# Kernel tuning notes

Hardware: AMD Instinct MI355X
Metric: run time of the kernel (lower is better)

The kernel has to match this reference:

```python
import jax, jax.numpy as jnp
import numpy as np

DEPTH, HEADS, DIM_HEAD, DIM, MLP, PATCH_DIM, NP_, NC = 8, 8, 64, 512, 2048, 512, 1024, 2
INNER = HEADS * DIM_HEAD
SCALE = DIM_HEAD ** -0.5
EPS = 1e-5

def layernorm(x, s, b):
    m = x.mean(-1, keepdims=True)
    v = ((x - m) ** 2).mean(-1, keepdims=True)
    return (x - m) * jax.lax.rsqrt(v + EPS) * s + b

def setup_inputs() -> dict:
    key = jax.random.key(0)
    ks = jax.random.split(key, 24)
    g = lambda k, sh, sc=0.02: jax.random.normal(k, sh, dtype=jnp.float32) * sc
    return {
        "img": jax.random.normal(ks[0], (4, NP_, PATCH_DIM), dtype=jnp.float32),
        "embed_w": g(ks[1], (PATCH_DIM, DIM)), "embed_b": jnp.zeros((DIM,), jnp.float32),
        "pos_emb": g(ks[2], (1, NP_ + 1, DIM), 1.0), "cls_token": g(ks[3], (1, 1, DIM), 1.0),
        "ln1_s": jnp.ones((DEPTH, DIM), jnp.float32), "ln1_b": jnp.zeros((DEPTH, DIM), jnp.float32),
        "qkv_w": g(ks[4], (DEPTH, DIM, 3 * INNER)),
        "out_w": g(ks[5], (DEPTH, INNER, DIM)), "out_b": jnp.zeros((DEPTH, DIM), jnp.float32),
        "ln2_s": jnp.ones((DEPTH, DIM), jnp.float32), "ln2_b": jnp.zeros((DEPTH, DIM), jnp.float32),
        "ff_w1": g(ks[6], (DEPTH, DIM, MLP)), "ff_b1": jnp.zeros((DEPTH, MLP), jnp.float32),
        "ff_w2": g(ks[7], (DEPTH, MLP, DIM)), "ff_b2": jnp.zeros((DEPTH, DIM), jnp.float32),
        "head_ln_s": jnp.ones((DIM,), jnp.float32), "head_ln_b": jnp.zeros((DIM,), jnp.float32),
        "head_w": g(ks[8], (DIM, NC)), "head_b": jnp.zeros((NC,), jnp.float32),
    }

def reference(img, embed_w, embed_b, pos_emb, cls_token, ln1_s, ln1_b, qkv_w, out_w, out_b,
              ln2_s, ln2_b, ff_w1, ff_b1, ff_w2, ff_b2, head_ln_s, head_ln_b, head_w, head_b):
    B, N, _ = img.shape
    x = img @ embed_w + embed_b                       # [B, N, DIM]
    cls = jnp.broadcast_to(cls_token, (B, 1, DIM))
    x = jnp.concatenate([cls, x], axis=1) + pos_emb[:, :N + 1]
    for l in range(DEPTH):
        h = layernorm(x, ln1_s[l], ln1_b[l])
        qkv = h @ qkv_w[l]                            # [B, N+1, 3*INNER]
        q, k, v = jnp.split(qkv, 3, axis=-1)
        rh = lambda t: t.reshape(B, N + 1, HEADS, DIM_HEAD).transpose(0, 2, 1, 3)
        q, k, v = rh(q), rh(k), rh(v)                 # [B, H, N+1, Dh]
        dots = jnp.einsum('bhnd,bhmd->bhnm', q, k) * SCALE
        attn = jax.nn.softmax(dots, axis=-1)
        o = jnp.einsum('bhnm,bhmd->bhnd', attn, v)
        o = o.transpose(0, 2, 1, 3).reshape(B, N + 1, INNER)
        x = o @ out_w[l] + out_b[l] + x
        h = layernorm(x, ln2_s[l], ln2_b[l])
        h = jax.nn.gelu(h @ ff_w1[l] + ff_b1[l], approximate=False)
        x = h @ ff_w2[l] + ff_b2[l] + x
    x = x[:, 0]                                       # cls pooling
    x = layernorm(x, head_ln_s, head_ln_b)
    return (jax.nn.sigmoid(x @ head_w + head_b),)
```

## Files before the change

kernel.cpp:

```cpp
#include <hip/hip_runtime.h>
#include <math.h>
#include <stdint.h>

#define NHEADS   8
#define DHEAD    64
#define DIMM     512
#define MLPD     2048
#define NPATCH   1024
#define NTOK     1025
#define BATCH    4
#define ROWS     (BATCH*NTOK)
#define TOKPAD   1088
#define ATT_SCALE 0.125f
#define LN_EPS   1e-5f

typedef __attribute__((ext_vector_type(8))) short short8;
typedef __attribute__((ext_vector_type(4))) float f32x4;

__device__ __forceinline__ unsigned short f2bf(float f) {
  union { float f; unsigned u; } c; c.f = f;
  unsigned u = c.u;
  return (unsigned short)((u + 0x7fffu + ((u >> 16) & 1u)) >> 16);
}

__device__ __forceinline__ float wsum(float v) {
#pragma unroll
  for (int o = 32; o > 0; o >>= 1) v += __shfl_xor(v, o, 64);
  return v;
}

__device__ __forceinline__ void gl_lds16(const void* g, const void* l) {
  __builtin_amdgcn_global_load_lds(
      (const __attribute__((address_space(1))) unsigned int*)(uintptr_t)g,
      (__attribute__((address_space(3))) unsigned int*)(unsigned int)(uintptr_t)l,
      16, 0, 0);
}

template <int TM, int TN, int WR, int WC>
__global__ __launch_bounds__(256) void mgemm_k(
    const unsigned short* __restrict__ A, const unsigned short* __restrict__ Bt,
    const float* __restrict__ bias, const float* __restrict__ res,
    void* __restrict__ Cout, int M, int N, int K, int flags)
{
  constexpr int AF = TM / WR / 16;
  constexpr int BF = TN / WC / 16;
  constexpr int AG = TM / 32;
  constexpr int BG = TN / 32;
  __shared__ unsigned short sA[2][TM * 64];
  __shared__ unsigned short sB[2][TN * 64];
  const int tid = threadIdx.x;
  const int w = tid >> 6, lane = tid & 63;
  const int quad = lane >> 4, l15 = lane & 15;
  const int m0 = blockIdx.y * TM, n0 = blockIdx.x * TN;
  const int wrow = (w / WC) * (TM / WR);
  const int wcol = (w % WC) * (TN / WC);
  const int lrow = lane >> 3;
  const int lkg = (lane & 7) ^ lrow;

  size_t abase[AG], bbase[BG];
#pragma unroll
  for (int g = 0; g < AG; g++) {
    int grp = w * AG + g;
    int ar = m0 + grp * 8 + lrow; ar = ar < M ? ar : M - 1;
    abase[g] = (size_t)ar * K + lkg * 8;
  }
#pragma unroll
  for (int g = 0; g < BG; g++) {
    int grp = w * BG + g;
    int br = n0 + grp * 8 + lrow;
    bbase[g] = (size_t)br * K + lkg * 8;
  }

  auto stage = [&](int k0, int buf) {
#pragma unroll
    for (int g = 0; g < AG; g++)
      gl_lds16(A + abase[g] + k0, &sA[buf][(w * AG + g) * 512]);
#pragma unroll
    for (int g = 0; g < BG; g++)
      gl_lds16(Bt + bbase[g] + k0, &sB[buf][(w * BG + g) * 512]);
  };

  f32x4 acc[AF][BF];
#pragma unroll
  for (int i = 0; i < AF; i++)
#pragma unroll
    for (int j = 0; j < BF; j++) { f32x4 z = {0.f, 0.f, 0.f, 0.f}; acc[i][j] = z; }

  stage(0, 0);
  const int nsteps = K >> 6;
  for (int step = 0; step < nsteps; step++) {
    const int buf = step & 1;
    __syncthreads();
    if (step + 1 < nsteps) stage((step + 1) << 6, buf ^ 1);
#pragma unroll
    for (int kk = 0; kk < 2; kk++) {
      short8 af[AF], bfr[BF];
#pragma unroll
      for (int i = 0; i < AF; i++) {
        int r = wrow + i * 16 + l15;
        af[i] = *(const short8*)&sA[buf][r * 64 + (((kk * 4 + quad) ^ (lane & 7)) << 3)];
      }
#pragma unroll
      for (int j = 0; j < BF; j++) {
        int r = wcol + j * 16 + l15;
        bfr[j] = *(const short8*)&sB[buf][r * 64 + (((kk * 4 + quad) ^ (lane & 7)) << 3)];
      }
#pragma unroll
      for (int i = 0; i < AF; i++)
#pragma unroll
        for (int j = 0; j < BF; j++)
          acc[i][j] = __builtin_amdgcn_mfma_f32_16x16x32_bf16(af[i], bfr[j], acc[i][j], 0, 0, 0);
    }
  }

  const bool do_gelu = flags & 1;
  const bool out_bf  = flags & 2;
#pragma unroll
  for (int i = 0; i < AF; i++) {
#pragma unroll
    for (int rg = 0; rg < 4; rg++) {
      int row = m0 + wrow + i * 16 + quad * 4 + rg;
      if (row >= M) continue;
#pragma unroll
      for (int j = 0; j < BF; j++) {
        int col = n0 + wcol + j * 16 + l15;
        float v = acc[i][j][rg];
        if (bias) v += bias[col];
        if (do_gelu) v = 0.5f * v * (1.0f + erff(v * 0.70710678118654752f));
        if (res) v += res[(size_t)row * N + col];
        if (out_bf) ((unsigned short*)Cout)[(size_t)row * N + col] = f2bf(v);
        else        ((float*)Cout)[(size_t)row * N + col] = v;
      }
    }
  }
}

__global__ __launch_bounds__(256) void vtrans_k(
    const unsigned short* __restrict__ qkv, unsigned short* __restrict__ vT)
{
  __shared__ unsigned short tile[64 * 64];
  const int bh = blockIdx.y, b = bh >> 3, h = bh & 7;
  const int t0 = blockIdx.x * 64;
  const int tid = threadIdx.x;
#pragma unroll
  for (int it = 0; it < 2; ++it) {
    int lin = it * 256 + tid;
    int tok = lin >> 3, dg = lin & 7;
    int gt = t0 + tok; gt = gt < NTOK ? gt : NTOK - 1;
    uint4 v = *(const uint4*)(qkv + (size_t)(b * NTOK + gt) * 1536 + 1024 + h * 64 + dg * 8);
    *(uint4*)&tile[tok * 64 + ((dg ^ (tok & 7)) << 3)] = v;
  }
  __syncthreads();
  unsigned short* outp = vT + ((size_t)bh * 64) * TOKPAD + t0;
#pragma unroll
  for (int it = 0; it < 2; ++it) {
    int lin = it * 256 + tid;
    int d = lin >> 3, tg = lin & 7;
    alignas(16) unsigned short o[8];
#pragma unroll
    for (int j = 0; j < 8; j++) {
      int tok = tg * 8 + j;
      o[j] = tile[tok * 64 + ((((d >> 3) ^ (tok & 7)) & 7) << 3) + (d & 7)];
    }
    *(uint4*)(outp + (size_t)d * TOKPAD + tg * 8) = *(const uint4*)o;
  }
}

__global__ __launch_bounds__(256) void attn_k(
    const unsigned short* __restrict__ qkv, const unsigned short* __restrict__ vT,
    unsigned short* __restrict__ out)
{
  __shared__ unsigned short qs[64 * 64];
  __shared__ unsigned short ps[64 * 64];
  __shared__ unsigned short ks[2][64 * 64];
  __shared__ unsigned short vs[2][64 * 64];
  const int bh = blockIdx.y, b = bh >> 3, h = bh & 7;
  const int q0 = blockIdx.x * 64;
  const int tid = threadIdx.x, w = tid >> 6, lane = tid & 63;
  const int quad = lane >> 4, l15 = lane & 15;
  const int lrow = lane >> 3, lkg = (lane & 7) ^ lrow;
  const unsigned short* qbase = qkv + (size_t)(b * NTOK) * 1536 + h * 64;
  const unsigned short* kbase = qbase + 512;
  const unsigned short* vtb   = vT + (size_t)bh * 64 * TOKPAD;

  auto stage_kv = [&](int c0, int buf) {
#pragma unroll
    for (int g = 0; g < 2; g++) {
      int grp = w * 2 + g;
      int tok = c0 + grp * 8 + lrow; tok = tok < NTOK ? tok : NTOK - 1;
      gl_lds16(kbase + (size_t)tok * 1536 + lkg * 8, &ks[buf][grp * 512]);
      int d = grp * 8 + lrow;
      gl_lds16(vtb + (size_t)d * TOKPAD + c0 + lkg * 8, &vs[buf][grp * 512]);
    }
  };

#pragma unroll
  for (int g = 0; g < 2; g++) {
    int grp = w * 2 + g;
    int tok = q0 + grp * 8 + lrow; tok = tok < NTOK ? tok : NTOK - 1;
    gl_lds16(qbase + (size_t)tok * 1536 + lkg * 8, &qs[grp * 512]);
  }
  stage_kv(0, 0);

  short8 ones;
#pragma unroll
  for (int i = 0; i < 8; i++) ones[i] = (short)0x3F80;

  f32x4 Oa[4];
#pragma unroll
  for (int n = 0; n < 4; n++) { f32x4 z = {0.f, 0.f, 0.f, 0.f}; Oa[n] = z; }
  float mst[4], lst[4];
#pragma unroll
  for (int r = 0; r < 4; r++) { mst[r] = -1e30f; lst[r] = 0.f; }

  const int nchunks = (NTOK + 63) / 64;
  for (int c = 0; c < nchunks; c++) {
    const int c0 = c * 64;
    const int buf = c & 1;
    __syncthreads();
    if (c + 1 < nchunks) stage_kv(c0 + 64, buf ^ 1);

    short8 aq[2];
#pragma unroll
    for (int kk = 0; kk < 2; kk++)
      aq[kk] = *(const short8*)&qs[(w * 16 + l15) * 64 + (((kk * 4 + quad) ^ (lane & 7)) << 3)];
    f32x4 sa[4];
#pragma unroll
    for (int n = 0; n < 4; n++) {
      f32x4 s = {0.f, 0.f, 0.f, 0.f};
#pragma unroll
      for (int kk = 0; kk < 2; kk++) {
        short8 bk = *(const short8*)&ks[buf][(n * 16 + l15) * 64 + (((kk * 4 + quad) ^ (lane & 7)) << 3)];
        s = __builtin_amdgcn_mfma_f32_16x16x32_bf16(aq[kk], bk, s, 0, 0, 0);
      }
      sa[n] = s;
    }

#pragma unroll
    for (int n = 0; n < 4; n++) {
      bool oob = (c0 + n * 16 + l15) >= NTOK;
#pragma unroll
      for (int rg = 0; rg < 4; rg++) {
        float sc = sa[n][rg] * ATT_SCALE;
        sa[n][rg] = oob ? -1e30f : sc;
      }
    }
    float alpha[4];
#pragma unroll
    for (int rg = 0; rg < 4; rg++) {
      float mx = fmaxf(fmaxf(sa[0][rg], sa[1][rg]), fmaxf(sa[2][rg], sa[3][rg]));
#pragma unroll
      for (int o = 1; o < 16; o <<= 1) mx = fmaxf(mx, __shfl_xor(mx, o, 64));
      float nm = fmaxf(mst[rg], mx);
      alpha[rg] = __expf(mst[rg] - nm);
      mst[rg] = nm;
#pragma unroll
      for (int n = 0; n < 4; n++) sa[n][rg] = __expf(sa[n][rg] - nm);
    }

#pragma unroll
    for (int n = 0; n < 4; n++)
#pragma unroll
      for (int rg = 0; rg < 4; rg++) {
        int row = w * 16 + quad * 4 + rg;
        int key = n * 16 + l15;
        ps[row * 64 + ((((key >> 3) ^ (row & 7)) & 7) << 3) + (key & 7)] = f2bf(sa[n][rg]);
      }

    short8 ap[2];
#pragma unroll
    for (int kk = 0; kk < 2; kk++)
      ap[kk] = *(const short8*)&ps[(w * 16 + l15) * 64 + (((kk * 4 + quad) ^ (lane & 7)) << 3)];

    f32x4 lsum = {0.f, 0.f, 0.f, 0.f};
#pragma unroll
    for (int kk = 0; kk < 2; kk++)
      lsum = __builtin_amdgcn_mfma_f32_16x16x32_bf16(ap[kk], ones, lsum, 0, 0, 0);

#pragma unroll
    for (int n = 0; n < 4; n++) {
      f32x4 o = Oa[n];
#pragma unroll
      for (int rg = 0; rg < 4; rg++) o[rg] *= alpha[rg];
#pragma unroll
      for (int kk = 0; kk < 2; kk++) {
        short8 bv = *(const short8*)&vs[buf][(n * 16 + l15) * 64 + (((kk * 4 + quad) ^ (lane & 7)) << 3)];
        o = __builtin_amdgcn_mfma_f32_16x16x32_bf16(ap[kk], bv, o, 0, 0, 0);
      }
      Oa[n] = o;
    }
#pragma unroll
    for (int rg = 0; rg < 4; rg++) lst[rg] = lst[rg] * alpha[rg] + lsum[rg];
  }

#pragma unroll
  for (int n = 0; n < 4; n++)
#pragma unroll
    for (int rg = 0; rg < 4; rg++) {
      int tok = q0 + w * 16 + quad * 4 + rg;
      if (tok < NTOK)
        out[(size_t)(b * NTOK + tok) * DIMM + h * 64 + n * 16 + l15] =
            f2bf(Oa[n][rg] / lst[rg]);
    }
}

__global__ __launch_bounds__(256) void ln_k(
    const float* __restrict__ X, const float* __restrict__ s,
    const float* __restrict__ b, unsigned short* __restrict__ Y, int nrows)
{
  const int w = threadIdx.x >> 6, lane = threadIdx.x & 63;
  const int row = blockIdx.x * 4 + w;
  if (row >= nrows) return;
  const float* x = X + (size_t)row * DIMM;
  float4 v0 = *(const float4*)(x + lane * 8);
  float4 v1 = *(const float4*)(x + lane * 8 + 4);
  float xv[8] = {v0.x, v0.y, v0.z, v0.w, v1.x, v1.y, v1.z, v1.w};
  float sum = 0.f, sq = 0.f;
#pragma unroll
  for (int i = 0; i < 8; i++) { sum += xv[i]; sq += xv[i] * xv[i]; }
  sum = wsum(sum); sq = wsum(sq);
  const float mean = sum * (1.0f / DIMM);
  const float var  = sq * (1.0f / DIMM) - mean * mean;
  const float r    = rsqrtf(var + LN_EPS);
  alignas(16) unsigned short tmp[8];
#pragma unroll
  for (int i = 0; i < 8; i++) {
    int d = lane * 8 + i;
    tmp[i] = f2bf((xv[i] - mean) * r * s[d] + b[d]);
  }
  *(uint4*)&Y[(size_t)row * DIMM + lane * 8] = *(const uint4*)tmp;
}

__global__ __launch_bounds__(256) void assemble_k(
    const float* __restrict__ emb, const float* __restrict__ cls,
    const float* __restrict__ pos, float* __restrict__ X)
{
  int idx = blockIdx.x * 256 + threadIdx.x;
  if (idx >= BATCH * NTOK * DIMM) return;
  int d = idx & (DIMM - 1);
  int t = (idx >> 9) % NTOK;
  int b = idx / (NTOK * DIMM);
  float v = (t == 0) ? cls[d] : emb[((size_t)b * NPATCH + (t - 1)) * DIMM + d];
  X[idx] = v + pos[(size_t)t * DIMM + d];
}

__global__ __launch_bounds__(256) void cast_k(
    const float* __restrict__ X, unsigned short* __restrict__ Y, int n4)
{
  int i = blockIdx.x * 256 + threadIdx.x;
  if (i >= n4) return;
  float4 v = ((const float4*)X)[i];
  alignas(8) unsigned short o[4] = {f2bf(v.x), f2bf(v.y), f2bf(v.z), f2bf(v.w)};
  ((uint2*)Y)[i] = *(const uint2*)o;
}

__global__ __launch_bounds__(256) void tcast_k(
    const float* __restrict__ W, unsigned short* __restrict__ Wt, int K, int N)
{
  __shared__ float t[32][33];
  const size_t off = (size_t)blockIdx.z * K * N;
  W += off; Wt += off;
  int n0 = blockIdx.x * 32, k0 = blockIdx.y * 32;
  int tx = threadIdx.x & 31, ty = threadIdx.x >> 5;
#pragma unroll
  for (int i = 0; i < 4; i++)
    t[ty + 8 * i][tx] = W[(size_t)(k0 + ty + 8 * i) * N + n0 + tx];
  __syncthreads();
#pragma unroll
  for (int i = 0; i < 4; i++) {
    int n = ty + 8 * i;
    Wt[(size_t)(n0 + n) * K + k0 + tx] = f2bf(t[tx][n]);
  }
}

__global__ __launch_bounds__(256) void head_k(
    const float* __restrict__ X, const float* __restrict__ s,
    const float* __restrict__ bln, const float* __restrict__ W,
    const float* __restrict__ bh, float* __restrict__ out)
{
  const int w = threadIdx.x >> 6, lane = threadIdx.x & 63;
  if (w >= BATCH) return;
  const float* x = X + (size_t)w * NTOK * DIMM;
  float4 v0 = *(const float4*)(x + lane * 8);
  float4 v1 = *(const float4*)(x + lane * 8 + 4);
  float xv[8] = {v0.x, v0.y, v0.z, v0.w, v1.x, v1.y, v1.z, v1.w};
  float sum = 0.f, sq = 0.f;
#pragma unroll
  for (int i = 0; i < 8; i++) { sum += xv[i]; sq += xv[i] * xv[i]; }
  sum = wsum(sum); sq = wsum(sq);
  const float mean = sum * (1.0f / DIMM);
  const float var  = sq * (1.0f / DIMM) - mean * mean;
  const float r    = rsqrtf(var + LN_EPS);
  float l0 = 0.f, l1 = 0.f;
#pragma unroll
  for (int i = 0; i < 8; i++) {
    int d = lane * 8 + i;
    float xn = (xv[i] - mean) * r * s[d] + bln[d];
    l0 = fmaf(xn, W[d * 2 + 0], l0);
    l1 = fmaf(xn, W[d * 2 + 1], l1);
  }
  l0 = wsum(l0); l1 = wsum(l1);
  if (lane == 0) {
    out[w * 2 + 0] = 1.0f / (1.0f + expf(-(l0 + bh[0])));
    out[w * 2 + 1] = 1.0f / (1.0f + expf(-(l1 + bh[1])));
  }
}

extern "C" void kernel_launch(void* const* d_in, const int* in_sizes, int n_in,
                              void* d_out, int out_size, void* d_ws, size_t ws_size,
                              hipStream_t stream)
{
  const float* img       = (const float*)d_in[0];
  const float* embed_w   = (const float*)d_in[1];
  const float* embed_b   = (const float*)d_in[2];
  const float* pos_emb   = (const float*)d_in[3];
  const float* cls_token = (const float*)d_in[4];
  const float* ln1_s     = (const float*)d_in[5];
  const float* ln1_b     = (const float*)d_in[6];
  const float* qkv_w     = (const float*)d_in[7];
  const float* out_w     = (const float*)d_in[8];
  const float* out_b     = (const float*)d_in[9];
  const float* ln2_s     = (const float*)d_in[10];
  const float* ln2_b     = (const float*)d_in[11];
  const float* ff_w1     = (const float*)d_in[12];
  const float* ff_b1     = (const float*)d_in[13];
  const float* ff_w2     = (const float*)d_in[14];
  const float* ff_b2     = (const float*)d_in[15];
  const float* head_ln_s = (const float*)d_in[16];
  const float* head_ln_b = (const float*)d_in[17];
  const float* head_w    = (const float*)d_in[18];
  const float* head_b    = (const float*)d_in[19];
  float* out = (float*)d_out;

  char* p = (char*)d_ws;
  auto alloc = [&](size_t bytes) { char* r = p; p += (bytes + 255) & ~(size_t)255; return r; };

  unsigned short* wt_embed = (unsigned short*)alloc((size_t)512 * 512 * 2);
  unsigned short* wt_qkv   = (unsigned short*)alloc((size_t)8 * 1536 * 512 * 2);
  unsigned short* wt_out   = (unsigned short*)alloc((size_t)8 * 512 * 512 * 2);
  unsigned short* wt_ff1   = (unsigned short*)alloc((size_t)8 * 2048 * 512 * 2);
  unsigned short* wt_ff2   = (unsigned short*)alloc((size_t)8 * 512 * 2048 * 2);
  unsigned short* img_bf   = (unsigned short*)alloc((size_t)4096 * 512 * 2);
  float*          x        = (float*)alloc((size_t)ROWS * DIMM * 4);
  unsigned short* h        = (unsigned short*)alloc((size_t)ROWS * DIMM * 2);
  unsigned short* vTb      = (unsigned short*)alloc((size_t)32 * 64 * TOKPAD * 2);
  char*           big      = alloc((size_t)ROWS * MLPD * 2);
  unsigned short* qkvb     = (unsigned short*)big;
  unsigned short* attn_out = (unsigned short*)(big + (size_t)ROWS * 1536 * 2);
  unsigned short* ffh      = (unsigned short*)big;
  float*          embuf    = (float*)big;

  dim3 blk(256);

  cast_k<<<(4096 * 512 / 4 + 255) / 256, blk, 0, stream>>>(img, img_bf, 4096 * 512 / 4);
  tcast_k<<<dim3(16, 16, 1), blk, 0, stream>>>(embed_w, wt_embed, 512, 512);
  tcast_k<<<dim3(48, 16, 8), blk, 0, stream>>>(qkv_w, wt_qkv, 512, 1536);
  tcast_k<<<dim3(16, 16, 8), blk, 0, stream>>>(out_w, wt_out, 512, 512);
  tcast_k<<<dim3(64, 16, 8), blk, 0, stream>>>(ff_w1, wt_ff1, 512, 2048);
  tcast_k<<<dim3(16, 64, 8), blk, 0, stream>>>(ff_w2, wt_ff2, 2048, 512);

  mgemm_k<64, 64, 2, 2><<<dim3(8, 64), blk, 0, stream>>>(
      img_bf, wt_embed, embed_b, nullptr, embuf, 4096, 512, 512, 0);
  assemble_k<<<(BATCH * NTOK * DIMM + 255) / 256, blk, 0, stream>>>(
      embuf, cls_token, pos_emb, x);

  const int mt64 = (ROWS + 63) / 64;
  for (int l = 0; l < 8; l++) {
    ln_k<<<(ROWS + 3) / 4, blk, 0, stream>>>(
        x, ln1_s + l * DIMM, ln1_b + l * DIMM, h, ROWS);
    mgemm_k<64, 128, 1, 4><<<dim3(12, mt64), blk, 0, stream>>>(
        h, wt_qkv + (size_t)l * 1536 * 512, nullptr, nullptr,
        qkvb, ROWS, 1536, 512, 2);
    vtrans_k<<<dim3(17, 32), blk, 0, stream>>>(qkvb, vTb);
    attn_k<<<dim3(17, 32), blk, 0, stream>>>(qkvb, vTb, attn_out);
    mgemm_k<64, 64, 2, 2><<<dim3(8, mt64), blk, 0, stream>>>(
        attn_out, wt_out + (size_t)l * 512 * 512, out_b + l * DIMM, x,
        x, ROWS, 512, 512, 0);
    ln_k<<<(ROWS + 3) / 4, blk, 0, stream>>>(
        x, ln2_s + l * DIMM, ln2_b + l * DIMM, h, ROWS);
    mgemm_k<64, 128, 1, 4><<<dim3(16, mt64), blk, 0, stream>>>(
        h, wt_ff1 + (size_t)l * 2048 * 512, ff_b1 + l * MLPD, nullptr,
        ffh, ROWS, 2048, 512, 1 | 2);
    mgemm_k<64, 64, 2, 2><<<dim3(8, mt64), blk, 0, stream>>>(
        ffh, wt_ff2 + (size_t)l * 512 * 2048, ff_b2 + l * DIMM, x,
        x, ROWS, 512, 2048, 0);
  }

  head_k<<<1, blk, 0, stream>>>(x, head_ln_s, head_ln_b, head_w, head_b, out);
}
```

Before: 1.399 ms.

## Split attention over key chunks with combine kernel; larger single-buffered FF1 tile

Attention is split into two key-range halves via a third grid dimension. Each half writes unnormalized bf16 partial outputs plus per-row max and sum, and a new combine kernel merges them. This doubles the attention block count to fill the GPU better, at the cost of extra memory traffic and a second launch. Q fragments are now loaded straight from global memory instead of through LDS. Separately, the GEMM gains a single-buffer option, and FF1 uses a 128x128 tile with it to get more reuse per block at the price of lost load/compute overlap.

```diff
diff --git a/kernel.cpp b/kernel.cpp
--- a/kernel.cpp
+++ b/kernel.cpp
@@ -11,6 +11,8 @@
 #define BATCH    4
 #define ROWS     (BATCH*NTOK)
 #define TOKPAD   1088
+#define NCHUNK   17
+#define CSPLIT   9
 #define ATT_SCALE 0.125f
 #define LN_EPS   1e-5f
 
@@ -21,6 +23,10 @@
   union { float f; unsigned u; } c; c.f = f;
   unsigned u = c.u;
   return (unsigned short)((u + 0x7fffu + ((u >> 16) & 1u)) >> 16);
+}
+__device__ __forceinline__ float bf2f(unsigned short b) {
+  union { unsigned u; float f; } c; c.u = (unsigned)b << 16;
+  return c.f;
 }
 
 __device__ __forceinline__ float wsum(float v) {
@@ -36,7 +42,7 @@
       16, 0, 0);
 }
 
-template <int TM, int TN, int WR, int WC>
+template <int TM, int TN, int WR, int WC, bool DBUF>
 __global__ __launch_bounds__(256) void mgemm_k(
     const unsigned short* __restrict__ A, const unsigned short* __restrict__ Bt,
     const float* __restrict__ bias, const float* __restrict__ res,
@@ -46,8 +52,9 @@
   constexpr int BF = TN / WC / 16;
   constexpr int AG = TM / 32;
   constexpr int BG = TN / 32;
-  __shared__ unsigned short sA[2][TM * 64];
-  __shared__ unsigned short sB[2][TN * 64];
+  constexpr int NB = DBUF ? 2 : 1;
+  __shared__ unsigned short sA[NB][TM * 64];
+  __shared__ unsigned short sB[NB][TN * 64];
   const int tid = threadIdx.x;
   const int w = tid >> 6, lane = tid & 63;
   const int quad = lane >> 4, l15 = lane & 15;
@@ -86,12 +93,7 @@
 #pragma unroll
     for (int j = 0; j < BF; j++) { f32x4 z = {0.f, 0.f, 0.f, 0.f}; acc[i][j] = z; }
 
-  stage(0, 0);
-  const int nsteps = K >> 6;
-  for (int step = 0; step < nsteps; step++) {
-    const int buf = step & 1;
-    __syncthreads();
-    if (step + 1 < nsteps) stage((step + 1) << 6, buf ^ 1);
+  auto compute = [&](int buf) {
 #pragma unroll
     for (int kk = 0; kk < 2; kk++) {
       short8 af[AF], bfr[BF];
@@ -110,6 +112,24 @@
 #pragma unroll
         for (int j = 0; j < BF; j++)
           acc[i][j] = __builtin_amdgcn_mfma_f32_16x16x32_bf16(af[i], bfr[j], acc[i][j], 0, 0, 0);
+    }
+  };
+
+  const int nsteps = K >> 6;
+  if constexpr (DBUF) {
+    stage(0, 0);
+    for (int step = 0; step < nsteps; step++) {
+      const int buf = step & 1;
+      __syncthreads();
+      if (step + 1 < nsteps) stage((step + 1) << 6, buf ^ 1);
+      compute(buf);
+    }
+  } else {
+    for (int step = 0; step < nsteps; step++) {
+      __syncthreads();
+      stage(step << 6, 0);
+      __syncthreads();
+      compute(0);
     }
   }
 
@@ -168,14 +188,14 @@
 
 __global__ __launch_bounds__(256) void attn_k(
     const unsigned short* __restrict__ qkv, const unsigned short* __restrict__ vT,
-    unsigned short* __restrict__ out)
-{
-  __shared__ unsigned short qs[64 * 64];
+    unsigned short* __restrict__ po, float* __restrict__ ml)
+{
   __shared__ unsigned short ps[64 * 64];
   __shared__ unsigned short ks[2][64 * 64];
   __shared__ unsigned short vs[2][64 * 64];
   const int bh = blockIdx.y, b = bh >> 3, h = bh & 7;
   const int q0 = blockIdx.x * 64;
+  const int split = blockIdx.z;
   const int tid = threadIdx.x, w = tid >> 6, lane = tid & 63;
   const int quad = lane >> 4, l15 = lane & 15;
   const int lrow = lane >> 3, lkg = (lane & 7) ^ lrow;
@@ -194,13 +214,15 @@
     }
   };
 
-#pragma unroll
-  for (int g = 0; g < 2; g++) {
-    int grp = w * 2 + g;
-    int tok = q0 + grp * 8 + lrow; tok = tok < NTOK ? tok : NTOK - 1;
-    gl_lds16(qbase + (size_t)tok * 1536 + lkg * 8, &qs[grp * 512]);
-  }
-  stage_kv(0, 0);
+  const int cbeg = split ? CSPLIT : 0;
+  const int cend = split ? NCHUNK : CSPLIT;
+  stage_kv(cbeg * 64, 0);
+
+  int qr = q0 + w * 16 + l15; qr = qr < NTOK ? qr : NTOK - 1;
+  const unsigned short* qrow = qbase + (size_t)qr * 1536;
+  short8 aq[2];
+  aq[0] = *(const short8*)(qrow + quad * 8);
+  aq[1] = *(const short8*)(qrow + 32 + quad * 8);
 
   short8 ones;
 #pragma unroll
@@ -213,17 +235,12 @@
 #pragma unroll
   for (int r = 0; r < 4; r++) { mst[r] = -1e30f; lst[r] = 0.f; }
 
-  const int nchunks = (NTOK + 63) / 64;
-  for (int c = 0; c < nchunks; c++) {
+  for (int c = cbeg; c < cend; c++) {
     const int c0 = c * 64;
-    const int buf = c & 1;
+    const int buf = (c - cbeg) & 1;
     __syncthreads();
-    if (c + 1 < nchunks) stage_kv(c0 + 64, buf ^ 1);
-
-    short8 aq[2];
-#pragma unroll
-    for (int kk = 0; kk < 2; kk++)
-      aq[kk] = *(const short8*)&qs[(w * 16 + l15) * 64 + (((kk * 4 + quad) ^ (lane & 7)) << 3)];
+    if (c + 1 < cend) stage_kv(c0 + 64, buf ^ 1);
+
     f32x4 sa[4];
 #pragma unroll
     for (int n = 0; n < 4; n++) {
@@ -293,15 +310,52 @@
     for (int rg = 0; rg < 4; rg++) lst[rg] = lst[rg] * alpha[rg] + lsum[rg];
   }
 
+  unsigned short* pob = po + (size_t)split * ROWS * DIMM;
 #pragma unroll
   for (int n = 0; n < 4; n++)
 #pragma unroll
     for (int rg = 0; rg < 4; rg++) {
       int tok = q0 + w * 16 + quad * 4 + rg;
       if (tok < NTOK)
-        out[(size_t)(b * NTOK + tok) * DIMM + h * 64 + n * 16 + l15] =
-            f2bf(Oa[n][rg] / lst[rg]);
-    }
+        pob[(size_t)(b * NTOK + tok) * DIMM + h * 64 + n * 16 + l15] = f2bf(Oa[n][rg]);
+    }
+  if (l15 == 0) {
+#pragma unroll
+    for (int rg = 0; rg < 4; rg++) {
+      int tok = q0 + w * 16 + quad * 4 + rg;
+      if (tok < NTOK) {
+        size_t mi = ((size_t)(split * 32 + bh) * NTOK + tok) * 2;
+        ml[mi] = mst[rg]; ml[mi + 1] = lst[rg];
+      }
+    }
+  }
+}
+
+__global__ __launch_bounds__(256) void acomb_k(
+    const unsigned short* __restrict__ po, const float* __restrict__ ml,
+    unsigned short* __restrict__ out)
+{
+  int idx = blockIdx.x * 256 + threadIdx.x;
+  if (idx >= ROWS * 64) return;
+  int row = idx >> 6, g = idx & 63;
+  int h = g >> 3;
+  int b = row / NTOK, tok = row - b * NTOK;
+  int bh = b * 8 + h;
+  size_t m0i = ((size_t)bh * NTOK + tok) * 2;
+  size_t m1i = ((size_t)(32 + bh) * NTOK + tok) * 2;
+  float m0 = ml[m0i], l0 = ml[m0i + 1];
+  float m1 = ml[m1i], l1 = ml[m1i + 1];
+  float M = fmaxf(m0, m1);
+  float w0 = __expf(m0 - M), w1 = __expf(m1 - M);
+  float inv = 1.0f / (w0 * l0 + w1 * l1);
+  size_t off = (size_t)row * DIMM + g * 8;
+  alignas(16) unsigned short a0[8], a1[8], o[8];
+  *(uint4*)a0 = *(const uint4*)(po + off);
+  *(uint4*)a1 = *(const uint4*)(po + (size_t)ROWS * DIMM + off);
+#pragma unroll
+  for (int i = 0; i < 8; i++)
+    o[i] = f2bf((w0 * bf2f(a0[i]) + w1 * bf2f(a1[i])) * inv);
+  *(uint4*)(out + off) = *(const uint4*)o;
 }
 
 __global__ __launch_bounds__(256) void ln_k(
@@ -444,6 +498,8 @@
   float*          x        = (float*)alloc((size_t)ROWS * DIMM * 4);
   unsigned short* h        = (unsigned short*)alloc((size_t)ROWS * DIMM * 2);
   unsigned short* vTb      = (unsigned short*)alloc((size_t)32 * 64 * TOKPAD * 2);
+  unsigned short* po       = (unsigned short*)alloc((size_t)2 * ROWS * DIMM * 2);
+  float*          mlb      = (float*)alloc((size_t)2 * 32 * NTOK * 2 * 4);
   char*           big      = alloc((size_t)ROWS * MLPD * 2);
   unsigned short* qkvb     = (unsigned short*)big;
   unsigned short* attn_out = (unsigned short*)(big + (size_t)ROWS * 1536 * 2);
@@ -459,29 +515,31 @@
   tcast_k<<<dim3(64, 16, 8), blk, 0, stream>>>(ff_w1, wt_ff1, 512, 2048);
   tcast_k<<<dim3(16, 64, 8), blk, 0, stream>>>(ff_w2, wt_ff2, 2048, 512);
 
-  mgemm_k<64, 64, 2, 2><<<dim3(8, 64), blk, 0, stream>>>(
+  mgemm_k<64, 64, 2, 2, true><<<dim3(8, 64), blk, 0, stream>>>(
       img_bf, wt_embed, embed_b, nullptr, embuf, 4096, 512, 512, 0);
   assemble_k<<<(BATCH * NTOK * DIMM + 255) / 256, blk, 0, stream>>>(
       embuf, cls_token, pos_emb, x);
 
-  const int mt64 = (ROWS + 63) / 64;
+  const int mt64  = (ROWS + 63) / 64;
+  const int mt128 = (ROWS + 127) / 128;
   for (int l = 0; l < 8; l++) {
     ln_k<<<(ROWS + 3) / 4, blk, 0, stream>>>(
         x, ln1_s + l * DIMM, ln1_b + l * DIMM, h, ROWS);
-    mgemm_k<64, 128, 1, 4><<<dim3(12, mt64), blk, 0, stream>>>(
+    mgemm_k<64, 128, 1, 4, true><<<dim3(12, mt64), blk, 0, stream>>>(
         h, wt_qkv + (size_t)l * 1536 * 512, nullptr, nullptr,
         qkvb, ROWS, 1536, 512, 2);
     vtrans_k<<<dim3(17, 32), blk, 0, stream>>>(qkvb, vTb);
-    attn_k<<<dim3(17, 32), blk, 0, stream>>>(qkvb, vTb, attn_out);
-    mgemm_k<64, 64, 2, 2><<<dim3(8, mt64), blk, 0, stream>>>(
+    attn_k<<<dim3(17, 32, 2), blk, 0, stream>>>(qkvb, vTb, po, mlb);
+    acomb_k<<<(ROWS * 64 + 255) / 256, blk, 0, stream>>>(po, mlb, attn_out);
+    mgemm_k<64, 64, 2, 2, true><<<dim3(8, mt64), blk, 0, stream>>>(
         attn_out, wt_out + (size_t)l * 512 * 512, out_b + l * DIMM, x,
         x, ROWS, 512, 512, 0);
     ln_k<<<(ROWS + 3) / 4, blk, 0, stream>>>(
         x, ln2_s + l * DIMM, ln2_b + l * DIMM, h, ROWS);
-    mgemm_k<64, 128, 1, 4><<<dim3(16, mt64), blk, 0, stream>>>(
+    mgemm_k<128, 128, 2, 2, false><<<dim3(16, mt128), blk, 0, stream>>>(
         h, wt_ff1 + (size_t)l * 2048 * 512, ff_b1 + l * MLPD, nullptr,
         ffh, ROWS, 2048, 512, 1 | 2);
-    mgemm_k<64, 64, 2, 2><<<dim3(8, mt64), blk, 0, stream>>>(
+    mgemm_k<64, 64, 2, 2, true><<<dim3(8, mt64), blk, 0, stream>>>(
         ffh, wt_ff2 + (size_t)l * 512 * 2048, ff_b2 + l * DIMM, x,
         x, ROWS, 512, 2048, 0);
   }
```

New measurement: 1.481 ms. +5.9%, slower.
